# Kernel optimization log

Hardware: AMD Instinct MI355X
Metric: run time of the kernel (lower is better)

Reference implementation:

```python
import jax, jax.numpy as jnp
import numpy as np

S = 256          # image_size
NEAR = 0.1       # NMR default near plane
FAR = 100.0      # NMR default far plane / background depth
CHUNK = 16       # faces per scan step (memory control)
EYE_Z = -1.0 / np.tan(np.radians(30.0))  # camera_mode='look', viewing_angle=30


def _render(verts, faces):
    """Orthographic rasterizer matching NMR forward: silhouette + depth.

    verts: [B,N,3] float, faces: [F,3] int (shared across batch).
    """
    B = verts.shape[0]
    # NMR forward flips the y axis, then the 'look' camera (default direction
    # [0,0,1], up [0,1,0]) reduces to a translation by -eye.
    v = verts * jnp.array([1.0, -1.0, 1.0], verts.dtype)
    v = v - jnp.array([0.0, 0.0, EYE_Z], verts.dtype)

    F = faces.shape[0]
    pad = (-F) % CHUNK
    # padded faces are (0,0,0) -> zero-area triangles, rejected by the area test
    faces_p = jnp.concatenate([faces, jnp.zeros((pad, 3), faces.dtype)], 0)
    nch = faces_p.shape[0] // CHUNK
    fv = v[:, faces_p]                                  # [B, Fp, 3, 3]
    fv = jnp.moveaxis(fv.reshape(B, nch, CHUNK, 3, 3), 1, 0)  # [nch, B, C, 3, 3]

    # NMR pixel-center convention: x_p = (2*xi + 1 - S)/S, row 0 at +y (top)
    xs = (2.0 * jnp.arange(S, dtype=verts.dtype) + 1.0 - S) / S
    px = xs[None, None, None, :]          # [1,1,1,W]
    py = (-xs)[None, None, :, None]       # [1,1,H,1]

    def body(zbuf, fvc):                  # fvc: [B, C, 3, 3]
        x, y, z = fvc[..., 0], fvc[..., 1], fvc[..., 2]
        x0, x1, x2 = x[..., 0], x[..., 1], x[..., 2]
        y0, y1, y2 = y[..., 0], y[..., 1], y[..., 2]
        z0, z1, z2 = z[..., 0], z[..., 1], z[..., 2]
        # signed area*2; dividing edge functions by it handles both windings
        area = (x1 - x0) * (y2 - y0) - (x2 - x0) * (y1 - y0)      # [B,C]
        ok = jnp.abs(area) > 1e-7
        inv_area = jnp.where(ok, 1.0 / jnp.where(ok, area, 1.0), 0.0)[..., None, None]

        def edge(xa, ya, xb, yb):
            # signed area of (p, a, b), expanded as linear function of (px,py)
            a = xa * yb - xb * ya
            b = ya - yb
            c = xb - xa
            return a[..., None, None] + b[..., None, None] * px + c[..., None, None] * py

        w0 = edge(x1, y1, x2, y2) * inv_area        # [B,C,H,W]
        w1 = edge(x2, y2, x0, y0) * inv_area
        w2 = 1.0 - w0 - w1
        inside = (w0 >= 0) & (w1 >= 0) & (w2 >= 0) & ok[..., None, None]
        # perspective-correct depth interpolation as in NMR's rasterizer
        zinv = (w0 / z0[..., None, None] + w1 / z1[..., None, None]
                + w2 / z2[..., None, None])
        zq = 1.0 / jnp.maximum(zinv, 1e-8)
        cand = jnp.where(inside & (zq > NEAR) & (zq < FAR), zq, FAR)
        return jnp.minimum(zbuf, cand.min(axis=1)), None

    zbuf0 = jnp.full((B, S, S), FAR, verts.dtype)
    zbuf, _ = jax.lax.scan(body, zbuf0, fv)
    sil = (zbuf < FAR).astype(verts.dtype)
    return sil, zbuf


def setup_inputs() -> dict:
    key = jax.random.key(0)
    k1, k2, k3 = jax.random.split(key, 3)
    B, N, F = 16, 778, 1538
    xy = jax.random.uniform(k1, (B, N, 2), minval=-0.8, maxval=0.8)
    z = jax.random.uniform(k2, (B, N, 1), minval=-0.5, maxval=0.8)
    verts = jnp.concatenate([xy, z], axis=-1).astype(jnp.float32)
    faces = jax.random.randint(k3, (F, 3), 0, N, dtype=jnp.int32)
    return {"verts": verts, "faces": faces}


def reference(verts, faces):
    # returns (silhouettes [B,H,W], depth [B,H,W]) like NMR.forward(depth=True)
    return _render(verts, faces)
```

## Files before the change

kernel.cpp:

```cpp
#include <hip/hip_runtime.h>
#include <stdint.h>

#define SS 256
#define FAR_F 100.0f
#define REG 32
#define NREG 64
#define NCH 3
#define CAPP 448
#define CAPQ 448
#define CAPF 120
#define OVN  96
#define DEFN 32

struct __align__(16) PackedCoef {
    float4 q0;
    float4 q1;
    float4 q2;
};

__global__ void nmr_prep(const float* __restrict__ verts,
                         const int* __restrict__ faces,
                         PackedCoef* __restrict__ pc,
                         uint32_t* __restrict__ bbx,
                         int B, int N, int F)
{
#pragma clang fp contract(off)
    int idx = blockIdx.x * blockDim.x + threadIdx.x;
    if (idx >= B * F) return;
    int b = idx / F;
    int f = idx - b * F;

    int i0 = faces[3 * f + 0], i1 = faces[3 * f + 1], i2 = faces[3 * f + 2];
    const float* vb = verts + (size_t)(3 * N) * b;
    const float EZ = -1.7320508075688772f;

    float x0 = vb[3 * i0 + 0], y0 = -vb[3 * i0 + 1], z0 = vb[3 * i0 + 2] - EZ;
    float x1 = vb[3 * i1 + 0], y1 = -vb[3 * i1 + 1], z1 = vb[3 * i1 + 2] - EZ;
    float x2 = vb[3 * i2 + 0], y2 = -vb[3 * i2 + 1], z2 = vb[3 * i2 + 2] - EZ;

    float area = (x1 - x0) * (y2 - y0) - (x2 - x0) * (y1 - y0);
    bool ok = fabsf(area) > 1e-7f;
    float ia = ok ? (1.0f / area) : 0.0f;

    float A0 = (x1 * y2 - x2 * y1) * ia, B0 = (y1 - y2) * ia, C0 = (x2 - x1) * ia;
    float A1 = (x2 * y0 - x0 * y2) * ia, B1 = (y2 - y0) * ia, C1 = (x0 - x2) * ia;
    float rz0 = 1.0f / z0, rz1 = 1.0f / z1, rz2 = 1.0f / z2;
    float d0 = rz0 - rz2, d1 = rz1 - rz2;
    float Z0 = rz2 + A0 * d0 + A1 * d1;
    float Zx = B0 * d0 + B1 * d1;
    float Zy = C0 * d0 + C1 * d1;
    float S = fabsf(A0) + fabsf(B0) + fabsf(C0) + fabsf(A1) + fabsf(B1) + fabsf(C1) + 1.0f;
    float ef = 3e-6f * S;

    uint32_t bb = 255u | (0u << 8) | (255u << 16) | (0u << 24);
    if (ok) {
        float xmn = fminf(x0, fminf(x1, x2)), xmx = fmaxf(x0, fmaxf(x1, x2));
        float ymn = fminf(y0, fminf(y1, y2)), ymx = fmaxf(y0, fmaxf(y1, y2));
        int jlo = (int)floorf(128.0f * (xmn + 1.0f) - 0.5f) - 1;
        int jhi = (int)ceilf (128.0f * (xmx + 1.0f) - 0.5f) + 1;
        int ilo = (int)floorf((255.0f - 256.0f * ymx) * 0.5f) - 1;
        int ihi = (int)ceilf ((255.0f - 256.0f * ymn) * 0.5f) + 1;
        jlo = max(0, min(255, jlo)); jhi = max(0, min(255, jhi));
        ilo = max(0, min(255, ilo)); ihi = max(0, min(255, ihi));
        if (jhi >= jlo && ihi >= ilo)
            bb = (uint32_t)jlo | ((uint32_t)jhi << 8) | ((uint32_t)ilo << 16) | ((uint32_t)ihi << 24);
    }

    PackedCoef c;
    c.q0 = make_float4(A0, B0, C0, A1);
    c.q1 = make_float4(B1, C1, Zx, Zy);
    c.q2 = make_float4(Z0, ef, __uint_as_float(bb), __uint_as_float((uint32_t)f));
    pc[idx] = c;
    bbx[idx] = bb;
}

__device__ __forceinline__ void exact_body(
    float4 q1, float4 q2,
    float px, float py0, float py1, float py2, float py3,
    const float* __restrict__ verts, const int* __restrict__ faces, int N, int b,
    float& best0, float& best1, float& best2, float& best3)
{
#pragma clang fp contract(off)
    float zbv = __builtin_fmaf(q1.z, px, q2.x);
    float zi0 = __builtin_fmaf(q1.w, py0, zbv);
    float zi1 = __builtin_fmaf(q1.w, py1, zbv);
    float zi2 = __builtin_fmaf(q1.w, py2, zbv);
    float zi3 = __builtin_fmaf(q1.w, py3, zbv);
    int fid = __builtin_amdgcn_readfirstlane((int)__float_as_uint(q2.w));
    int i0f = faces[3 * fid + 0], i1f = faces[3 * fid + 1], i2f = faces[3 * fid + 2];
    const float* vb = verts + (size_t)(3 * N) * b;
    float x0 = vb[3 * i0f + 0], y0 = -vb[3 * i0f + 1];
    float x1 = vb[3 * i1f + 0], y1 = -vb[3 * i1f + 1];
    float x2 = vb[3 * i2f + 0], y2 = -vb[3 * i2f + 1];
    float area = (x1 - x0) * (y2 - y0) - (x2 - x0) * (y1 - y0);
    float ia = 1.0f / area;
    float a0 = x1 * y2 - x2 * y1, b0e = y1 - y2, c0e = x2 - x1;
    float a1 = x2 * y0 - x0 * y2, b1e = y2 - y0, c1e = x0 - x2;
    float e0b = a0 + b0e * px;
    float e1b = a1 + b1e * px;
    { float u0 = (e0b + c0e * py0) * ia, u1 = (e1b + c1e * py0) * ia;
      if (fminf(u0, fminf(u1, (1.0f - u0) - u1)) >= 0.0f) best0 = fmaxf(best0, zi0); }
    { float u0 = (e0b + c0e * py1) * ia, u1 = (e1b + c1e * py1) * ia;
      if (fminf(u0, fminf(u1, (1.0f - u0) - u1)) >= 0.0f) best1 = fmaxf(best1, zi1); }
    { float u0 = (e0b + c0e * py2) * ia, u1 = (e1b + c1e * py2) * ia;
      if (fminf(u0, fminf(u1, (1.0f - u0) - u1)) >= 0.0f) best2 = fmaxf(best2, zi2); }
    { float u0 = (e0b + c0e * py3) * ia, u1 = (e1b + c1e * py3) * ia;
      if (fminf(u0, fminf(u1, (1.0f - u0) - u1)) >= 0.0f) best3 = fmaxf(best3, zi3); }
}

__device__ __forceinline__ void face_body(
    float4 q0, float4 q1, float4 q2,
    float px, float py0, float py1, float py2, float py3,
    const float* __restrict__ verts, const int* __restrict__ faces, int N, int b,
    float& best0, float& best1, float& best2, float& best3)
{
#pragma clang fp contract(off)
    const float ef = q2.y;
    float w0b = __builtin_fmaf(q0.y, px, q0.x);
    float w1b = __builtin_fmaf(q1.x, px, q0.w);
    float zbv = __builtin_fmaf(q1.z, px, q2.x);
    float w0_0 = __builtin_fmaf(q0.z, py0, w0b), w1_0 = __builtin_fmaf(q1.y, py0, w1b);
    float w0_1 = __builtin_fmaf(q0.z, py1, w0b), w1_1 = __builtin_fmaf(q1.y, py1, w1b);
    float w0_2 = __builtin_fmaf(q0.z, py2, w0b), w1_2 = __builtin_fmaf(q1.y, py2, w1b);
    float w0_3 = __builtin_fmaf(q0.z, py3, w0b), w1_3 = __builtin_fmaf(q1.y, py3, w1b);
    float m0 = fminf(w0_0, fminf(w1_0, (1.0f - w0_0) - w1_0));
    float m1 = fminf(w0_1, fminf(w1_1, (1.0f - w0_1) - w1_1));
    float m2 = fminf(w0_2, fminf(w1_2, (1.0f - w0_2) - w1_2));
    float m3 = fminf(w0_3, fminf(w1_3, (1.0f - w0_3) - w1_3));
    float zi0 = __builtin_fmaf(q1.w, py0, zbv);
    float zi1 = __builtin_fmaf(q1.w, py1, zbv);
    float zi2 = __builtin_fmaf(q1.w, py2, zbv);
    float zi3 = __builtin_fmaf(q1.w, py3, zbv);
    bool amb = (fabsf(m0) <= ef) | (fabsf(m1) <= ef) | (fabsf(m2) <= ef) | (fabsf(m3) <= ef);
    if (__any(amb)) {
        exact_body(q1, q2, px, py0, py1, py2, py3, verts, faces, N, b, best0, best1, best2, best3);
        return;
    }
    best0 = (m0 > ef) ? fmaxf(best0, zi0) : best0;
    best1 = (m1 > ef) ? fmaxf(best1, zi1) : best1;
    best2 = (m2 > ef) ? fmaxf(best2, zi2) : best2;
    best3 = (m3 > ef) ? fmaxf(best3, zi3) : best3;
}

__device__ __forceinline__ float wave_min_f(float x) {
    #pragma unroll
    for (int m = 1; m < 64; m <<= 1) x = fminf(x, __shfl_xor(x, m));
    return x;
}

__global__ __launch_bounds__(256, 5) void nmr_raster(
    const PackedCoef* __restrict__ pc,
    const uint32_t* __restrict__ bbx,
    const float* __restrict__ verts,
    const int* __restrict__ faces,
    uint32_t* __restrict__ zu,
    int B, int N, int F, int CH)
{
#pragma clang fp contract(off)
    __shared__ float4   pool[3 * CAPP];
    __shared__ __align__(16) uint32_t qlist[4][CAPQ];
    __shared__ int qcnt[4];
    __shared__ float4   fullr[CAPF];
    __shared__ __align__(16) float fkey[CAPF + 16];
    __shared__ uint16_t ovl[OVN];
    __shared__ uint16_t dlist[4][DEFN];
    __shared__ int cnt_p, cnt_f, cnt_o;

    const int tid = threadIdx.x;
    const int bid = blockIdx.x;
    const int ch = bid % NCH; int t = bid / NCH;
    const int reg = t % NREG; const int b = t / NREG;
    const int rj0 = (reg & 7) * REG;
    const int ri0 = (reg >> 3) * REG;

    if (tid == 0) { cnt_p = 0; cnt_f = 0; cnt_o = 0; }
    if (tid < 4) qcnt[tid] = 0;
    __syncthreads();

    const int f0 = ch * CH, f1 = min(F, f0 + CH);
    const uint32_t* bb = bbx + (size_t)b * F;
    const PackedCoef* pb = pc + (size_t)b * F;

    const float cxa = (float)(2 * rj0 + 1 - SS) * (1.0f / SS);
    const float cxb = (float)(2 * (rj0 + REG - 1) + 1 - SS) * (1.0f / SS);
    const float cya = (float)(SS - 1 - 2 * ri0) * (1.0f / SS);
    const float cyb = (float)(SS - 1 - 2 * (ri0 + REG - 1)) * (1.0f / SS);

    for (int f = f0 + tid; f < f1; f += 256) {
        uint32_t v = bb[f];
        int jlo = v & 255, jhi = (v >> 8) & 255, ilo = (v >> 16) & 255, ihi = (int)(v >> 24);
        if (jlo > rj0 + REG - 1 || jhi < rj0 || ilo > ri0 + REG - 1 || ihi < ri0) continue;
        PackedCoef P = pb[f];
        float b0a = __builtin_fmaf(P.q0.y, cxa, P.q0.x), b0b = __builtin_fmaf(P.q0.y, cxb, P.q0.x);
        float w0aa = __builtin_fmaf(P.q0.z, cya, b0a), w0ab = __builtin_fmaf(P.q0.z, cyb, b0a);
        float w0ba = __builtin_fmaf(P.q0.z, cya, b0b), w0bb = __builtin_fmaf(P.q0.z, cyb, b0b);
        float b1a = __builtin_fmaf(P.q1.x, cxa, P.q0.w), b1b = __builtin_fmaf(P.q1.x, cxb, P.q0.w);
        float w1aa = __builtin_fmaf(P.q1.y, cya, b1a), w1ab = __builtin_fmaf(P.q1.y, cyb, b1a);
        float w1ba = __builtin_fmaf(P.q1.y, cya, b1b), w1bb = __builtin_fmaf(P.q1.y, cyb, b1b);
        float w2aa = (1.0f - w0aa) - w1aa, w2ab = (1.0f - w0ab) - w1ab;
        float w2ba = (1.0f - w0ba) - w1ba, w2bb = (1.0f - w0bb) - w1bb;

        float m0n = fminf(fminf(w0aa, w0ab), fminf(w0ba, w0bb));
        float m0x = fmaxf(fmaxf(w0aa, w0ab), fmaxf(w0ba, w0bb));
        float m1n = fminf(fminf(w1aa, w1ab), fminf(w1ba, w1bb));
        float m1x = fmaxf(fmaxf(w1aa, w1ab), fmaxf(w1ba, w1bb));
        float m2n = fminf(fminf(w2aa, w2ab), fminf(w2ba, w2bb));
        float m2x = fmaxf(fmaxf(w2aa, w2ab), fmaxf(w2ba, w2bb));

        float Rm = 2.0f * P.q2.y;
        if (m0x < -Rm || m1x < -Rm || m2x < -Rm) continue;

        float za = __builtin_fmaf(P.q1.z, cxa, P.q2.x), zbq = __builtin_fmaf(P.q1.z, cxb, P.q2.x);
        float z_aa = __builtin_fmaf(P.q1.w, cya, za),  z_ab = __builtin_fmaf(P.q1.w, cyb, za);
        float z_ba = __builtin_fmaf(P.q1.w, cya, zbq), z_bb = __builtin_fmaf(P.q1.w, cyb, zbq);
        float cmax = fmaxf(fmaxf(z_aa, z_ab), fmaxf(z_ba, z_bb));
        float key = fmaxf(cmax + __builtin_fmaf(fabsf(cmax), 1e-6f, 1e-5f), 0.0f);

        bool full = (m0n > Rm && m1n > Rm && m2n > Rm);
        if (full) {
            int q = atomicAdd(&cnt_f, 1);
            if (q < CAPF) {
                fullr[q] = make_float4(P.q2.x, P.q1.z, P.q1.w, key);
                fkey[q] = key;
                continue;
            }
        }
        int p = atomicAdd(&cnt_p, 1);
        if (p < CAPP) {
            pool[3 * p + 0] = P.q0; pool[3 * p + 1] = P.q1; pool[3 * p + 2] = P.q2;
            uint32_t entry = ((__float_as_uint(key) + 0xFFFu) & 0xFFFFF000u) | (uint32_t)p;
            bool jx0 = (jlo <= rj0 + 15) && (jhi >= rj0);
            bool jx1 = (jlo <= rj0 + 31) && (jhi >= rj0 + 16);
            bool iy0 = (ilo <= ri0 + 15) && (ihi >= ri0);
            bool iy1 = (ilo <= ri0 + 31) && (ihi >= ri0 + 16);
            if (jx0 && iy0) { int s = atomicAdd(&qcnt[0], 1); qlist[0][s] = entry; }
            if (jx1 && iy0) { int s = atomicAdd(&qcnt[1], 1); qlist[1][s] = entry; }
            if (jx0 && iy1) { int s = atomicAdd(&qcnt[2], 1); qlist[2][s] = entry; }
            if (jx1 && iy1) { int s = atomicAdd(&qcnt[3], 1); qlist[3][s] = entry; }
        } else {
            int o = atomicAdd(&cnt_o, 1);
            if (o < OVN) ovl[o] = (uint16_t)f;
        }
    }
    __syncthreads();

    const int nf = min(cnt_f, CAPF), no = min(cnt_o, OVN);
    const int nf16 = (nf + 15) & ~15;
    for (int i = nf + tid; i < nf16; i += 256) fkey[i] = 0.0f;
    for (int q = 0; q < 4; ++q) {
        int n = qcnt[q]; int n4 = (n + 3) & ~3;
        for (int i = n + tid; i < n4; i += 256) qlist[q][i] = 0u;
    }
    __syncthreads();

    const int lane = tid & 63, w = tid >> 6;
    const int wj0 = rj0 + ((w & 1) << 4);
    const int wi0 = ri0 + ((w >> 1) << 4);
    const int j = wj0 + (lane & 15);
    const int i0r = wi0 + (lane >> 4);
    const float px = (float)(2 * j + 1 - SS) * (1.0f / SS);
    const float py0 = (float)(SS - 1 - 2 * (i0r + 0))  * (1.0f / SS);
    const float py1 = (float)(SS - 1 - 2 * (i0r + 4))  * (1.0f / SS);
    const float py2 = (float)(SS - 1 - 2 * (i0r + 8))  * (1.0f / SS);
    const float py3 = (float)(SS - 1 - 2 * (i0r + 12)) * (1.0f / SS);

    float best0 = 0.0f, best1 = 0.0f, best2 = 0.0f, best3 = 0.0f;

    for (int base = 0; base < nf16; base += 16) {
        float lm = wave_min_f(fminf(fminf(best0, best1), fminf(best2, best3)));
        for (int g = base; g < base + 16; g += 4) {
            float4 kk = *reinterpret_cast<const float4*>(&fkey[g]);
            float gmax = fmaxf(fmaxf(kk.x, kk.y), fmaxf(kk.z, kk.w));
            if (gmax <= lm) continue;
            #pragma unroll
            for (int u = 0; u < 4; ++u) {
                float key = (u == 0) ? kk.x : (u == 1) ? kk.y : (u == 2) ? kk.z : kk.w;
                if (key <= lm) continue;
                float4 z = fullr[g + u];
                float zb = __builtin_fmaf(z.y, px, z.x);
                best0 = fmaxf(best0, __builtin_fmaf(z.z, py0, zb));
                best1 = fmaxf(best1, __builtin_fmaf(z.z, py1, zb));
                best2 = fmaxf(best2, __builtin_fmaf(z.z, py2, zb));
                best3 = fmaxf(best3, __builtin_fmaf(z.z, py3, zb));
            }
        }
    }

    int dcnt = 0;
    const uint32_t* ql = &qlist[w][0];
    const int nq = qcnt[w];
    const int nq4 = (nq + 3) & ~3;
    for (int base = 0; base < nq4; base += 16) {
        float lm = wave_min_f(fminf(fminf(best0, best1), fminf(best2, best3)));
        uint32_t lmU = __float_as_uint(lm);
        int gend = min(base + 16, nq4);
        for (int g = base; g < gend; g += 4) {
            uint4 kk = *reinterpret_cast<const uint4*>(&ql[g]);
            uint32_t k0 = kk.x & 0xFFFFF000u, k1 = kk.y & 0xFFFFF000u;
            uint32_t k2 = kk.z & 0xFFFFF000u, k3 = kk.w & 0xFFFFF000u;
            uint32_t gmax = max(max(k0, k1), max(k2, k3));
            if (gmax <= lmU) continue;
            #pragma unroll
            for (int u = 0; u < 4; ++u) {
                uint32_t e = (u == 0) ? kk.x : (u == 1) ? kk.y : (u == 2) ? kk.z : kk.w;
                if ((e & 0xFFFFF000u) <= lmU) continue;
                int k = (int)(e & 0xFFFu);
                float4 q0 = pool[3 * k + 0];
                float4 q1 = pool[3 * k + 1];
                float4 q2 = pool[3 * k + 2];
                const float ef = q2.y;
                float w0b = __builtin_fmaf(q0.y, px, q0.x);
                float w1b = __builtin_fmaf(q1.x, px, q0.w);
                float zbv = __builtin_fmaf(q1.z, px, q2.x);
                float w0_0 = __builtin_fmaf(q0.z, py0, w0b), w1_0 = __builtin_fmaf(q1.y, py0, w1b);
                float w0_1 = __builtin_fmaf(q0.z, py1, w0b), w1_1 = __builtin_fmaf(q1.y, py1, w1b);
                float w0_2 = __builtin_fmaf(q0.z, py2, w0b), w1_2 = __builtin_fmaf(q1.y, py2, w1b);
                float w0_3 = __builtin_fmaf(q0.z, py3, w0b), w1_3 = __builtin_fmaf(q1.y, py3, w1b);
                float m0 = fminf(w0_0, fminf(w1_0, (1.0f - w0_0) - w1_0));
                float m1 = fminf(w0_1, fminf(w1_1, (1.0f - w0_1) - w1_1));
                float m2 = fminf(w0_2, fminf(w1_2, (1.0f - w0_2) - w1_2));
                float m3 = fminf(w0_3, fminf(w1_3, (1.0f - w0_3) - w1_3));
                float zi0 = __builtin_fmaf(q1.w, py0, zbv);
                float zi1 = __builtin_fmaf(q1.w, py1, zbv);
                float zi2 = __builtin_fmaf(q1.w, py2, zbv);
                float zi3 = __builtin_fmaf(q1.w, py3, zbv);
                best0 = (m0 > ef) ? fmaxf(best0, zi0) : best0;
                best1 = (m1 > ef) ? fmaxf(best1, zi1) : best1;
                best2 = (m2 > ef) ? fmaxf(best2, zi2) : best2;
                best3 = (m3 > ef) ? fmaxf(best3, zi3) : best3;
                float mabs = fminf(fminf(fabsf(m0), fabsf(m1)), fminf(fabsf(m2), fabsf(m3)));
                if (__any(mabs <= ef)) {
                    if (dcnt == DEFN) {
                        for (int d = 0; d < dcnt; ++d) {
                            int kk2 = (int)dlist[w][d];
                            exact_body(pool[3 * kk2 + 1], pool[3 * kk2 + 2],
                                       px, py0, py1, py2, py3, verts, faces, N, b,
                                       best0, best1, best2, best3);
                        }
                        dcnt = 0;
                    }
                    if (lane == 0) dlist[w][dcnt] = (uint16_t)k;
                    dcnt++;
                }
            }
        }
    }
    for (int d = 0; d < dcnt; ++d) {
        int kk2 = (int)dlist[w][d];
        exact_body(pool[3 * kk2 + 1], pool[3 * kk2 + 2],
                   px, py0, py1, py2, py3, verts, faces, N, b,
                   best0, best1, best2, best3);
    }

    for (int k = 0; k < no; ++k) {
        int fid = __builtin_amdgcn_readfirstlane((int)ovl[k]);
        float4 q2 = pb[fid].q2;
        uint32_t bv = __float_as_uint(q2.z);
        int jlo = bv & 255, jhi = (bv >> 8) & 255, ilo = (bv >> 16) & 255, ihi = (int)(bv >> 24);
        if (jlo > wj0 + 15 || jhi < wj0 || ilo > wi0 + 15 || ihi < wi0) continue;
        face_body(pb[fid].q0, pb[fid].q1, q2,
                  px, py0, py1, py2, py3, verts, faces, N, b,
                  best0, best1, best2, best3);
    }

    const size_t base = (size_t)b * (SS * SS) + (size_t)i0r * SS + j;
    if (best0 > 0.0f) atomicMin(&zu[base + 0 * 4 * SS], __float_as_uint(1.0f / best0));
    if (best1 > 0.0f) atomicMin(&zu[base + 1 * 4 * SS], __float_as_uint(1.0f / best1));
    if (best2 > 0.0f) atomicMin(&zu[base + 2 * 4 * SS], __float_as_uint(1.0f / best2));
    if (best3 > 0.0f) atomicMin(&zu[base + 3 * 4 * SS], __float_as_uint(1.0f / best3));
}

__global__ void nmr_final(float* __restrict__ out, int B)
{
    int idx = blockIdx.x * 256 + threadIdx.x;
    if (idx >= B * SS * SS) return;
    uint32_t* zu = (uint32_t*)(out + (size_t)B * SS * SS);
    uint32_t u = zu[idx];
    bool cov = (u != 0xFFFFFFFFu);
    out[idx] = cov ? 1.0f : 0.0f;
    ((float*)zu)[idx] = cov ? __uint_as_float(u) : FAR_F;
}

extern "C" void kernel_launch(void* const* d_in, const int* in_sizes, int n_in,
                              void* d_out, int out_size, void* d_ws, size_t ws_size,
                              hipStream_t stream)
{
    const float* verts = (const float*)d_in[0];
    const int*   faces = (const int*)d_in[1];
    float* out = (float*)d_out;

    const int B = out_size / (2 * SS * SS);
    const int F = in_sizes[1] / 3;
    const int N = in_sizes[0] / (3 * B);

    PackedCoef* pc = (PackedCoef*)d_ws;
    uint32_t*  bbx = (uint32_t*)((char*)d_ws + (size_t)B * F * sizeof(PackedCoef));
    uint32_t*  zu  = (uint32_t*)(out + (size_t)B * SS * SS);

    hipMemsetAsync(zu, 0xFF, (size_t)B * SS * SS * sizeof(uint32_t), stream);

    const int total = B * F;
    nmr_prep<<<(total + 255) / 256, 256, 0, stream>>>(verts, faces, pc, bbx, B, N, F);

    const int CH = (F + NCH - 1) / NCH;
    nmr_raster<<<B * NREG * NCH, 256, 0, stream>>>(pc, bbx, verts, faces, zu, B, N, F, CH);

    nmr_final<<<(B * SS * SS + 255) / 256, 256, 0, stream>>>(out, B);
}
```

Measured before the change: 88.05 us.

## Classify faces per quadrant with separate full-cover lists and compact pool

Binning now tests each face against every 16x16 quadrant separately, using separable edge-function bounds, rather than against the whole 32x32 region. Faces that fully cover a quadrant go into per-quadrant full lists, which lets more faces take the cheap depth-only path. The pool entry shrinks to two float4 plus a packed (Z0, face id, half-precision epsilon) word, which frees shared memory. Launch bounds drop from 5 to 4 blocks per CU, and the fp16 epsilon with a small safety factor may slightly change the ambiguity classification.

Measured after the change: 78.01 us. -11.4%, faster.

```diff
diff --git a/kernel.cpp b/kernel.cpp
--- a/kernel.cpp
+++ b/kernel.cpp
@@ -1,4 +1,5 @@
 #include <hip/hip_runtime.h>
+#include <hip/hip_fp16.h>
 #include <stdint.h>
 
 #define SS 256
@@ -7,8 +8,8 @@
 #define NREG 64
 #define NCH 3
 #define CAPP 448
-#define CAPQ 448
-#define CAPF 120
+#define CAPQ 352
+#define CAPFQ 224
 #define OVN  96
 #define DEFN 32
 
@@ -75,18 +76,18 @@
 }
 
 __device__ __forceinline__ void exact_body(
-    float4 q1, float4 q2,
+    float Zx, float Zy, float Z0, int fid,
     float px, float py0, float py1, float py2, float py3,
     const float* __restrict__ verts, const int* __restrict__ faces, int N, int b,
     float& best0, float& best1, float& best2, float& best3)
 {
 #pragma clang fp contract(off)
-    float zbv = __builtin_fmaf(q1.z, px, q2.x);
-    float zi0 = __builtin_fmaf(q1.w, py0, zbv);
-    float zi1 = __builtin_fmaf(q1.w, py1, zbv);
-    float zi2 = __builtin_fmaf(q1.w, py2, zbv);
-    float zi3 = __builtin_fmaf(q1.w, py3, zbv);
-    int fid = __builtin_amdgcn_readfirstlane((int)__float_as_uint(q2.w));
+    float zbv = __builtin_fmaf(Zx, px, Z0);
+    float zi0 = __builtin_fmaf(Zy, py0, zbv);
+    float zi1 = __builtin_fmaf(Zy, py1, zbv);
+    float zi2 = __builtin_fmaf(Zy, py2, zbv);
+    float zi3 = __builtin_fmaf(Zy, py3, zbv);
+    fid = __builtin_amdgcn_readfirstlane(fid);
     int i0f = faces[3 * fid + 0], i1f = faces[3 * fid + 1], i2f = faces[3 * fid + 2];
     const float* vb = verts + (size_t)(3 * N) * b;
     float x0 = vb[3 * i0f + 0], y0 = -vb[3 * i0f + 1];
@@ -133,7 +134,8 @@
     float zi3 = __builtin_fmaf(q1.w, py3, zbv);
     bool amb = (fabsf(m0) <= ef) | (fabsf(m1) <= ef) | (fabsf(m2) <= ef) | (fabsf(m3) <= ef);
     if (__any(amb)) {
-        exact_body(q1, q2, px, py0, py1, py2, py3, verts, faces, N, b, best0, best1, best2, best3);
+        exact_body(q1.z, q1.w, q2.x, (int)__float_as_uint(q2.w),
+                   px, py0, py1, py2, py3, verts, faces, N, b, best0, best1, best2, best3);
         return;
     }
     best0 = (m0 > ef) ? fmaxf(best0, zi0) : best0;
@@ -148,7 +150,7 @@
     return x;
 }
 
-__global__ __launch_bounds__(256, 5) void nmr_raster(
+__global__ __launch_bounds__(256, 4) void nmr_raster(
     const PackedCoef* __restrict__ pc,
     const uint32_t* __restrict__ bbx,
     const float* __restrict__ verts,
@@ -157,14 +159,13 @@
     int B, int N, int F, int CH)
 {
 #pragma clang fp contract(off)
-    __shared__ float4   pool[3 * CAPP];
-    __shared__ __align__(16) uint32_t qlist[4][CAPQ];
-    __shared__ int qcnt[4];
-    __shared__ float4   fullr[CAPF];
-    __shared__ __align__(16) float fkey[CAPF + 16];
+    __shared__ float4   pool[2 * CAPP];
+    __shared__ uint2    zef[CAPP];
+    __shared__ float4   qfull[4][CAPFQ];
+    __shared__ __align__(16) uint32_t qpart[4][CAPQ];
     __shared__ uint16_t ovl[OVN];
     __shared__ uint16_t dlist[4][DEFN];
-    __shared__ int cnt_p, cnt_f, cnt_o;
+    __shared__ int qcnt[4], qfcnt[4], cnt_p, cnt_o;
 
     const int tid = threadIdx.x;
     const int bid = blockIdx.x;
@@ -173,83 +174,121 @@
     const int rj0 = (reg & 7) * REG;
     const int ri0 = (reg >> 3) * REG;
 
-    if (tid == 0) { cnt_p = 0; cnt_f = 0; cnt_o = 0; }
-    if (tid < 4) qcnt[tid] = 0;
+    if (tid == 0) { cnt_p = 0; cnt_o = 0; }
+    if (tid < 4) { qcnt[tid] = 0; qfcnt[tid] = 0; }
     __syncthreads();
 
     const int f0 = ch * CH, f1 = min(F, f0 + CH);
     const uint32_t* bb = bbx + (size_t)b * F;
     const PackedCoef* pb = pc + (size_t)b * F;
 
-    const float cxa = (float)(2 * rj0 + 1 - SS) * (1.0f / SS);
-    const float cxb = (float)(2 * (rj0 + REG - 1) + 1 - SS) * (1.0f / SS);
-    const float cya = (float)(SS - 1 - 2 * ri0) * (1.0f / SS);
-    const float cyb = (float)(SS - 1 - 2 * (ri0 + REG - 1)) * (1.0f / SS);
+    const float cx0 = (float)(2 * rj0 + 1 - SS) * (1.0f / SS);
+    const float cx1 = (float)(2 * (rj0 + 15) + 1 - SS) * (1.0f / SS);
+    const float cx2 = (float)(2 * (rj0 + 16) + 1 - SS) * (1.0f / SS);
+    const float cx3 = (float)(2 * (rj0 + 31) + 1 - SS) * (1.0f / SS);
+    const float cy0 = (float)(SS - 1 - 2 * ri0) * (1.0f / SS);
+    const float cy1 = (float)(SS - 1 - 2 * (ri0 + 15)) * (1.0f / SS);
+    const float cy2 = (float)(SS - 1 - 2 * (ri0 + 16)) * (1.0f / SS);
+    const float cy3 = (float)(SS - 1 - 2 * (ri0 + 31)) * (1.0f / SS);
 
     for (int f = f0 + tid; f < f1; f += 256) {
         uint32_t v = bb[f];
         int jlo = v & 255, jhi = (v >> 8) & 255, ilo = (v >> 16) & 255, ihi = (int)(v >> 24);
         if (jlo > rj0 + REG - 1 || jhi < rj0 || ilo > ri0 + REG - 1 || ihi < ri0) continue;
         PackedCoef P = pb[f];
-        float b0a = __builtin_fmaf(P.q0.y, cxa, P.q0.x), b0b = __builtin_fmaf(P.q0.y, cxb, P.q0.x);
-        float w0aa = __builtin_fmaf(P.q0.z, cya, b0a), w0ab = __builtin_fmaf(P.q0.z, cyb, b0a);
-        float w0ba = __builtin_fmaf(P.q0.z, cya, b0b), w0bb = __builtin_fmaf(P.q0.z, cyb, b0b);
-        float b1a = __builtin_fmaf(P.q1.x, cxa, P.q0.w), b1b = __builtin_fmaf(P.q1.x, cxb, P.q0.w);
-        float w1aa = __builtin_fmaf(P.q1.y, cya, b1a), w1ab = __builtin_fmaf(P.q1.y, cyb, b1a);
-        float w1ba = __builtin_fmaf(P.q1.y, cya, b1b), w1bb = __builtin_fmaf(P.q1.y, cyb, b1b);
-        float w2aa = (1.0f - w0aa) - w1aa, w2ab = (1.0f - w0ab) - w1ab;
-        float w2ba = (1.0f - w0ba) - w1ba, w2bb = (1.0f - w0bb) - w1bb;
-
-        float m0n = fminf(fminf(w0aa, w0ab), fminf(w0ba, w0bb));
-        float m0x = fmaxf(fmaxf(w0aa, w0ab), fmaxf(w0ba, w0bb));
-        float m1n = fminf(fminf(w1aa, w1ab), fminf(w1ba, w1bb));
-        float m1x = fmaxf(fmaxf(w1aa, w1ab), fmaxf(w1ba, w1bb));
-        float m2n = fminf(fminf(w2aa, w2ab), fminf(w2ba, w2bb));
-        float m2x = fmaxf(fmaxf(w2aa, w2ab), fmaxf(w2ba, w2bb));
-
-        float Rm = 2.0f * P.q2.y;
-        if (m0x < -Rm || m1x < -Rm || m2x < -Rm) continue;
-
-        float za = __builtin_fmaf(P.q1.z, cxa, P.q2.x), zbq = __builtin_fmaf(P.q1.z, cxb, P.q2.x);
-        float z_aa = __builtin_fmaf(P.q1.w, cya, za),  z_ab = __builtin_fmaf(P.q1.w, cyb, za);
-        float z_ba = __builtin_fmaf(P.q1.w, cya, zbq), z_bb = __builtin_fmaf(P.q1.w, cyb, zbq);
-        float cmax = fmaxf(fmaxf(z_aa, z_ab), fmaxf(z_ba, z_bb));
-        float key = fmaxf(cmax + __builtin_fmaf(fabsf(cmax), 1e-6f, 1e-5f), 0.0f);
-
-        bool full = (m0n > Rm && m1n > Rm && m2n > Rm);
-        if (full) {
-            int q = atomicAdd(&cnt_f, 1);
-            if (q < CAPF) {
-                fullr[q] = make_float4(P.q2.x, P.q1.z, P.q1.w, key);
-                fkey[q] = key;
-                continue;
+        const float A0 = P.q0.x, B0 = P.q0.y, C0 = P.q0.z;
+        const float A1 = P.q0.w, B1 = P.q1.x, C1 = P.q1.y;
+        const float Zx = P.q1.z, Zy = P.q1.w, Z0 = P.q2.x, ef = P.q2.y;
+        const float A2 = (1.0f - A0) - A1, B2 = (0.0f - B0) - B1, C2 = (0.0f - C0) - C1;
+        const float Rm = 2.0f * ef;
+
+        float bn[3][2], bX[3][2], tn[3][2], tX[3][2];
+        {
+            float e_b0, e_b1, e_b2, e_b3, e_t0, e_t1, e_t2, e_t3;
+            e_b0 = __builtin_fmaf(B0, cx0, A0); e_b1 = __builtin_fmaf(B0, cx1, A0);
+            e_b2 = __builtin_fmaf(B0, cx2, A0); e_b3 = __builtin_fmaf(B0, cx3, A0);
+            e_t0 = C0 * cy0; e_t1 = C0 * cy1; e_t2 = C0 * cy2; e_t3 = C0 * cy3;
+            bn[0][0] = fminf(e_b0, e_b1); bX[0][0] = fmaxf(e_b0, e_b1);
+            bn[0][1] = fminf(e_b2, e_b3); bX[0][1] = fmaxf(e_b2, e_b3);
+            tn[0][0] = fminf(e_t0, e_t1); tX[0][0] = fmaxf(e_t0, e_t1);
+            tn[0][1] = fminf(e_t2, e_t3); tX[0][1] = fmaxf(e_t2, e_t3);
+            e_b0 = __builtin_fmaf(B1, cx0, A1); e_b1 = __builtin_fmaf(B1, cx1, A1);
+            e_b2 = __builtin_fmaf(B1, cx2, A1); e_b3 = __builtin_fmaf(B1, cx3, A1);
+            e_t0 = C1 * cy0; e_t1 = C1 * cy1; e_t2 = C1 * cy2; e_t3 = C1 * cy3;
+            bn[1][0] = fminf(e_b0, e_b1); bX[1][0] = fmaxf(e_b0, e_b1);
+            bn[1][1] = fminf(e_b2, e_b3); bX[1][1] = fmaxf(e_b2, e_b3);
+            tn[1][0] = fminf(e_t0, e_t1); tX[1][0] = fmaxf(e_t0, e_t1);
+            tn[1][1] = fminf(e_t2, e_t3); tX[1][1] = fmaxf(e_t2, e_t3);
+            e_b0 = __builtin_fmaf(B2, cx0, A2); e_b1 = __builtin_fmaf(B2, cx1, A2);
+            e_b2 = __builtin_fmaf(B2, cx2, A2); e_b3 = __builtin_fmaf(B2, cx3, A2);
+            e_t0 = C2 * cy0; e_t1 = C2 * cy1; e_t2 = C2 * cy2; e_t3 = C2 * cy3;
+            bn[2][0] = fminf(e_b0, e_b1); bX[2][0] = fmaxf(e_b0, e_b1);
+            bn[2][1] = fminf(e_b2, e_b3); bX[2][1] = fmaxf(e_b2, e_b3);
+            tn[2][0] = fminf(e_t0, e_t1); tX[2][0] = fmaxf(e_t0, e_t1);
+            tn[2][1] = fminf(e_t2, e_t3); tX[2][1] = fmaxf(e_t2, e_t3);
+        }
+        float zb0 = __builtin_fmaf(Zx, cx0, Z0), zb1 = __builtin_fmaf(Zx, cx1, Z0);
+        float zb2 = __builtin_fmaf(Zx, cx2, Z0), zb3 = __builtin_fmaf(Zx, cx3, Z0);
+        float zt0 = Zy * cy0, zt1 = Zy * cy1, zt2 = Zy * cy2, zt3 = Zy * cy3;
+        float zbX0 = fmaxf(zb0, zb1), zbX1 = fmaxf(zb2, zb3);
+        float ztX0 = fmaxf(zt0, zt1), ztX1 = fmaxf(zt2, zt3);
+
+        int partMask = 0;
+        float key0f = 0.0f, key1f = 0.0f, key2f = 0.0f, key3f = 0.0f;
+
+        #pragma unroll
+        for (int q = 0; q < 4; ++q) {
+            const int qx = q & 1, qy = q >> 1;
+            const int qj0 = rj0 + qx * 16, qi0 = ri0 + qy * 16;
+            if (jlo > qj0 + 15 || jhi < qj0 || ilo > qi0 + 15 || ihi < qi0) continue;
+            float e0x = bX[0][qx] + tX[0][qy];
+            float e1x = bX[1][qx] + tX[1][qy];
+            float e2x = bX[2][qx] + tX[2][qy];
+            if (e0x < -Rm || e1x < -Rm || e2x < -Rm) continue;
+            float km = (qx ? zbX1 : zbX0) + (qy ? ztX1 : ztX0);
+            float key = fmaxf(km + __builtin_fmaf(fabsf(km), 1e-6f, 1e-5f), 0.0f);
+            float e0n = bn[0][qx] + tn[0][qy];
+            float e1n = bn[1][qx] + tn[1][qy];
+            float e2n = bn[2][qx] + tn[2][qy];
+            bool full = (e0n > Rm) && (e1n > Rm) && (e2n > Rm);
+            if (full) {
+                int s = atomicAdd(&qfcnt[q], 1);
+                if (s < CAPFQ) { qfull[q][s] = make_float4(Z0, Zx, Zy, key); continue; }
+            }
+            partMask |= 1 << q;
+            if (q == 0) key0f = key; else if (q == 1) key1f = key;
+            else if (q == 2) key2f = key; else key3f = key;
+        }
+
+        if (partMask) {
+            int p = atomicAdd(&cnt_p, 1);
+            if (p < CAPP) {
+                pool[2 * p + 0] = P.q0;
+                pool[2 * p + 1] = P.q1;
+                uint32_t efh = (uint32_t)__half_as_ushort(__float2half(ef * 1.002f));
+                zef[p] = make_uint2(__float_as_uint(Z0), ((uint32_t)f << 16) | efh);
+                #pragma unroll
+                for (int q = 0; q < 4; ++q) {
+                    if (!((partMask >> q) & 1)) continue;
+                    float key = (q == 0) ? key0f : (q == 1) ? key1f : (q == 2) ? key2f : key3f;
+                    uint32_t entry = ((__float_as_uint(key) + 0xFFFu) & 0xFFFFF000u) | (uint32_t)p;
+                    int s = atomicAdd(&qcnt[q], 1);
+                    if (s < CAPQ) qpart[q][s] = entry;
+                    else { int o = atomicAdd(&cnt_o, 1); if (o < OVN) ovl[o] = (uint16_t)f; }
+                }
+            } else {
+                int o = atomicAdd(&cnt_o, 1);
+                if (o < OVN) ovl[o] = (uint16_t)f;
             }
         }
-        int p = atomicAdd(&cnt_p, 1);
-        if (p < CAPP) {
-            pool[3 * p + 0] = P.q0; pool[3 * p + 1] = P.q1; pool[3 * p + 2] = P.q2;
-            uint32_t entry = ((__float_as_uint(key) + 0xFFFu) & 0xFFFFF000u) | (uint32_t)p;
-            bool jx0 = (jlo <= rj0 + 15) && (jhi >= rj0);
-            bool jx1 = (jlo <= rj0 + 31) && (jhi >= rj0 + 16);
-            bool iy0 = (ilo <= ri0 + 15) && (ihi >= ri0);
-            bool iy1 = (ilo <= ri0 + 31) && (ihi >= ri0 + 16);
-            if (jx0 && iy0) { int s = atomicAdd(&qcnt[0], 1); qlist[0][s] = entry; }
-            if (jx1 && iy0) { int s = atomicAdd(&qcnt[1], 1); qlist[1][s] = entry; }
-            if (jx0 && iy1) { int s = atomicAdd(&qcnt[2], 1); qlist[2][s] = entry; }
-            if (jx1 && iy1) { int s = atomicAdd(&qcnt[3], 1); qlist[3][s] = entry; }
-        } else {
-            int o = atomicAdd(&cnt_o, 1);
-            if (o < OVN) ovl[o] = (uint16_t)f;
-        }
     }
     __syncthreads();
 
-    const int nf = min(cnt_f, CAPF), no = min(cnt_o, OVN);
-    const int nf16 = (nf + 15) & ~15;
-    for (int i = nf + tid; i < nf16; i += 256) fkey[i] = 0.0f;
+    const int no = min(cnt_o, OVN);
+    #pragma unroll
     for (int q = 0; q < 4; ++q) {
-        int n = qcnt[q]; int n4 = (n + 3) & ~3;
-        for (int i = n + tid; i < n4; i += 256) qlist[q][i] = 0u;
+        int n = min(qcnt[q], CAPQ); int n4 = (n + 3) & ~3;
+        for (int i = n + tid; i < n4; i += 256) qpart[q][i] = 0u;
     }
     __syncthreads();
 
@@ -266,108 +305,112 @@
 
     float best0 = 0.0f, best1 = 0.0f, best2 = 0.0f, best3 = 0.0f;
 
-    for (int base = 0; base < nf16; base += 16) {
-        float lm = wave_min_f(fminf(fminf(best0, best1), fminf(best2, best3)));
-        for (int g = base; g < base + 16; g += 4) {
-            float4 kk = *reinterpret_cast<const float4*>(&fkey[g]);
-            float gmax = fmaxf(fmaxf(kk.x, kk.y), fmaxf(kk.z, kk.w));
-            if (gmax <= lm) continue;
-            #pragma unroll
-            for (int u = 0; u < 4; ++u) {
-                float key = (u == 0) ? kk.x : (u == 1) ? kk.y : (u == 2) ? kk.z : kk.w;
-                if (key <= lm) continue;
-                float4 z = fullr[g + u];
-                float zb = __builtin_fmaf(z.y, px, z.x);
-                best0 = fmaxf(best0, __builtin_fmaf(z.z, py0, zb));
-                best1 = fmaxf(best1, __builtin_fmaf(z.z, py1, zb));
-                best2 = fmaxf(best2, __builtin_fmaf(z.z, py2, zb));
-                best3 = fmaxf(best3, __builtin_fmaf(z.z, py3, zb));
-            }
+    {
+        const float4* qf = &qfull[w][0];
+        const int nq = min(qfcnt[w], CAPFQ);
+        float lm = 0.0f;
+        for (int k = 0; k < nq; ++k) {
+            if ((k & 15) == 0) lm = wave_min_f(fminf(fminf(best0, best1), fminf(best2, best3)));
+            float4 z = qf[k];
+            if (z.w <= lm) continue;
+            float zb = __builtin_fmaf(z.y, px, z.x);
+            best0 = fmaxf(best0, __builtin_fmaf(z.z, py0, zb));
+            best1 = fmaxf(best1, __builtin_fmaf(z.z, py1, zb));
+            best2 = fmaxf(best2, __builtin_fmaf(z.z, py2, zb));
+            best3 = fmaxf(best3, __builtin_fmaf(z.z, py3, zb));
         }
     }
 
     int dcnt = 0;
-    const uint32_t* ql = &qlist[w][0];
-    const int nq = qcnt[w];
-    const int nq4 = (nq + 3) & ~3;
-    for (int base = 0; base < nq4; base += 16) {
-        float lm = wave_min_f(fminf(fminf(best0, best1), fminf(best2, best3)));
-        uint32_t lmU = __float_as_uint(lm);
-        int gend = min(base + 16, nq4);
-        for (int g = base; g < gend; g += 4) {
-            uint4 kk = *reinterpret_cast<const uint4*>(&ql[g]);
-            uint32_t k0 = kk.x & 0xFFFFF000u, k1 = kk.y & 0xFFFFF000u;
-            uint32_t k2 = kk.z & 0xFFFFF000u, k3 = kk.w & 0xFFFFF000u;
-            uint32_t gmax = max(max(k0, k1), max(k2, k3));
-            if (gmax <= lmU) continue;
-            #pragma unroll
-            for (int u = 0; u < 4; ++u) {
-                uint32_t e = (u == 0) ? kk.x : (u == 1) ? kk.y : (u == 2) ? kk.z : kk.w;
-                if ((e & 0xFFFFF000u) <= lmU) continue;
-                int k = (int)(e & 0xFFFu);
-                float4 q0 = pool[3 * k + 0];
-                float4 q1 = pool[3 * k + 1];
-                float4 q2 = pool[3 * k + 2];
-                const float ef = q2.y;
-                float w0b = __builtin_fmaf(q0.y, px, q0.x);
-                float w1b = __builtin_fmaf(q1.x, px, q0.w);
-                float zbv = __builtin_fmaf(q1.z, px, q2.x);
-                float w0_0 = __builtin_fmaf(q0.z, py0, w0b), w1_0 = __builtin_fmaf(q1.y, py0, w1b);
-                float w0_1 = __builtin_fmaf(q0.z, py1, w0b), w1_1 = __builtin_fmaf(q1.y, py1, w1b);
-                float w0_2 = __builtin_fmaf(q0.z, py2, w0b), w1_2 = __builtin_fmaf(q1.y, py2, w1b);
-                float w0_3 = __builtin_fmaf(q0.z, py3, w0b), w1_3 = __builtin_fmaf(q1.y, py3, w1b);
-                float m0 = fminf(w0_0, fminf(w1_0, (1.0f - w0_0) - w1_0));
-                float m1 = fminf(w0_1, fminf(w1_1, (1.0f - w0_1) - w1_1));
-                float m2 = fminf(w0_2, fminf(w1_2, (1.0f - w0_2) - w1_2));
-                float m3 = fminf(w0_3, fminf(w1_3, (1.0f - w0_3) - w1_3));
-                float zi0 = __builtin_fmaf(q1.w, py0, zbv);
-                float zi1 = __builtin_fmaf(q1.w, py1, zbv);
-                float zi2 = __builtin_fmaf(q1.w, py2, zbv);
-                float zi3 = __builtin_fmaf(q1.w, py3, zbv);
-                best0 = (m0 > ef) ? fmaxf(best0, zi0) : best0;
-                best1 = (m1 > ef) ? fmaxf(best1, zi1) : best1;
-                best2 = (m2 > ef) ? fmaxf(best2, zi2) : best2;
-                best3 = (m3 > ef) ? fmaxf(best3, zi3) : best3;
-                float mabs = fminf(fminf(fabsf(m0), fabsf(m1)), fminf(fabsf(m2), fabsf(m3)));
-                if (__any(mabs <= ef)) {
-                    if (dcnt == DEFN) {
-                        for (int d = 0; d < dcnt; ++d) {
-                            int kk2 = (int)dlist[w][d];
-                            exact_body(pool[3 * kk2 + 1], pool[3 * kk2 + 2],
-                                       px, py0, py1, py2, py3, verts, faces, N, b,
-                                       best0, best1, best2, best3);
+    {
+        const uint32_t* ql = &qpart[w][0];
+        const int nq = min(qcnt[w], CAPQ);
+        const int nq4 = (nq + 3) & ~3;
+        for (int base = 0; base < nq4; base += 16) {
+            float lm = wave_min_f(fminf(fminf(best0, best1), fminf(best2, best3)));
+            uint32_t lmU = __float_as_uint(lm);
+            int gend = min(base + 16, nq4);
+            for (int g = base; g < gend; g += 4) {
+                uint4 kk = *reinterpret_cast<const uint4*>(&ql[g]);
+                uint32_t k0 = kk.x & 0xFFFFF000u, k1 = kk.y & 0xFFFFF000u;
+                uint32_t k2 = kk.z & 0xFFFFF000u, k3 = kk.w & 0xFFFFF000u;
+                uint32_t gmax = max(max(k0, k1), max(k2, k3));
+                if (gmax <= lmU) continue;
+                #pragma unroll
+                for (int u = 0; u < 4; ++u) {
+                    uint32_t e = (u == 0) ? kk.x : (u == 1) ? kk.y : (u == 2) ? kk.z : kk.w;
+                    if ((e & 0xFFFFF000u) <= lmU) continue;
+                    int k = (int)(e & 0xFFFu);
+                    float4 q0 = pool[2 * k + 0];
+                    float4 q1 = pool[2 * k + 1];
+                    uint2  ze = zef[k];
+                    float Z0 = __uint_as_float(ze.x);
+                    float ef = __half2float(__ushort_as_half((unsigned short)(ze.y & 0xFFFFu)));
+                    float w0b = __builtin_fmaf(q0.y, px, q0.x);
+                    float w1b = __builtin_fmaf(q1.x, px, q0.w);
+                    float zbv = __builtin_fmaf(q1.z, px, Z0);
+                    float w0_0 = __builtin_fmaf(q0.z, py0, w0b), w1_0 = __builtin_fmaf(q1.y, py0, w1b);
+                    float w0_1 = __builtin_fmaf(q0.z, py1, w0b), w1_1 = __builtin_fmaf(q1.y, py1, w1b);
+                    float w0_2 = __builtin_fmaf(q0.z, py2, w0b), w1_2 = __builtin_fmaf(q1.y, py2, w1b);
+                    float w0_3 = __builtin_fmaf(q0.z, py3, w0b), w1_3 = __builtin_fmaf(q1.y, py3, w1b);
+                    float m0 = fminf(w0_0, fminf(w1_0, (1.0f - w0_0) - w1_0));
+                    float m1 = fminf(w0_1, fminf(w1_1, (1.0f - w0_1) - w1_1));
+                    float m2 = fminf(w0_2, fminf(w1_2, (1.0f - w0_2) - w1_2));
+                    float m3 = fminf(w0_3, fminf(w1_3, (1.0f - w0_3) - w1_3));
+                    float zi0 = __builtin_fmaf(q1.w, py0, zbv);
+                    float zi1 = __builtin_fmaf(q1.w, py1, zbv);
+                    float zi2 = __builtin_fmaf(q1.w, py2, zbv);
+                    float zi3 = __builtin_fmaf(q1.w, py3, zbv);
+                    best0 = (m0 > ef) ? fmaxf(best0, zi0) : best0;
+                    best1 = (m1 > ef) ? fmaxf(best1, zi1) : best1;
+                    best2 = (m2 > ef) ? fmaxf(best2, zi2) : best2;
+                    best3 = (m3 > ef) ? fmaxf(best3, zi3) : best3;
+                    float mabs = fminf(fminf(fabsf(m0), fabsf(m1)), fminf(fabsf(m2), fabsf(m3)));
+                    if (__any(mabs <= ef)) {
+                        if (dcnt == DEFN) {
+                            for (int d = 0; d < dcnt; ++d) {
+                                int kk2 = (int)dlist[w][d];
+                                float4 p1 = pool[2 * kk2 + 1];
+                                uint2  z2 = zef[kk2];
+                                exact_body(p1.z, p1.w, __uint_as_float(z2.x), (int)(z2.y >> 16),
+                                           px, py0, py1, py2, py3, verts, faces, N, b,
+                                           best0, best1, best2, best3);
+                            }
+                            dcnt = 0;
                         }
-                        dcnt = 0;
+                        if (lane == 0) dlist[w][dcnt] = (uint16_t)k;
+                        dcnt++;
                     }
-                    if (lane == 0) dlist[w][dcnt] = (uint16_t)k;
-                    dcnt++;
                 }
             }
         }
     }
     for (int d = 0; d < dcnt; ++d) {
         int kk2 = (int)dlist[w][d];
-        exact_body(pool[3 * kk2 + 1], pool[3 * kk2 + 2],
+        float4 p1 = pool[2 * kk2 + 1];
+        uint2  z2 = zef[kk2];
+        exact_body(p1.z, p1.w, __uint_as_float(z2.x), (int)(z2.y >> 16),
                    px, py0, py1, py2, py3, verts, faces, N, b,
                    best0, best1, best2, best3);
     }
 
+    const PackedCoef* pb2 = pc + (size_t)b * F;
     for (int k = 0; k < no; ++k) {
         int fid = __builtin_amdgcn_readfirstlane((int)ovl[k]);
-        float4 q2 = pb[fid].q2;
+        float4 q2 = pb2[fid].q2;
         uint32_t bv = __float_as_uint(q2.z);
         int jlo = bv & 255, jhi = (bv >> 8) & 255, ilo = (bv >> 16) & 255, ihi = (int)(bv >> 24);
         if (jlo > wj0 + 15 || jhi < wj0 || ilo > wi0 + 15 || ihi < wi0) continue;
-        face_body(pb[fid].q0, pb[fid].q1, q2,
+        face_body(pb2[fid].q0, pb2[fid].q1, q2,
                   px, py0, py1, py2, py3, verts, faces, N, b,
                   best0, best1, best2, best3);
     }
 
-    const size_t base = (size_t)b * (SS * SS) + (size_t)i0r * SS + j;
-    if (best0 > 0.0f) atomicMin(&zu[base + 0 * 4 * SS], __float_as_uint(1.0f / best0));
-    if (best1 > 0.0f) atomicMin(&zu[base + 1 * 4 * SS], __float_as_uint(1.0f / best1));
-    if (best2 > 0.0f) atomicMin(&zu[base + 2 * 4 * SS], __float_as_uint(1.0f / best2));
-    if (best3 > 0.0f) atomicMin(&zu[base + 3 * 4 * SS], __float_as_uint(1.0f / best3));
+    const size_t obase = (size_t)b * (SS * SS) + (size_t)i0r * SS + j;
+    if (best0 > 0.0f) atomicMin(&zu[obase + 0 * 4 * SS], __float_as_uint(1.0f / best0));
+    if (best1 > 0.0f) atomicMin(&zu[obase + 1 * 4 * SS], __float_as_uint(1.0f / best1));
+    if (best2 > 0.0f) atomicMin(&zu[obase + 2 * 4 * SS], __float_as_uint(1.0f / best2));
+    if (best3 > 0.0f) atomicMin(&zu[obase + 3 * 4 * SS], __float_as_uint(1.0f / best3));
 }
 
 __global__ void nmr_final(float* __restrict__ out, int B)
```
